# Optimization experiments

Hardware: AMD Instinct MI355X
Metric: run time of the kernel (lower is better)

Reference implementation:

```python
import jax, jax.numpy as jnp
import numpy as np
from jax import lax

B, C, H, W = 2, 3, 1024, 1024
SH, SW = 128, 128
FH, FW = H // SH, W // SW  # integer pooling factors (8, 8)
NPRE = 64
L = 0.24          # diffusion step size l
K = 0.03          # exp(log(0.03)), fixed logk for feature_extractor='none'
EPS = 1e-8
DEPS = 0.1


def _g(x):
    # g(x) = 1 / (1 + |x*x| / K^2)
    return 1.0 / (1.0 + (x * x) / (K * K))


def _conductance(feats):
    # cv: [B,1,H-1,W], ch: [B,1,H,W-1]; mean of |finite diff| over channels
    cv = _g(jnp.mean(jnp.abs(feats[:, :, 1:, :] - feats[:, :, :-1, :]), axis=1, keepdims=True))
    ch = _g(jnp.mean(jnp.abs(feats[:, :, :, 1:] - feats[:, :, :, :-1]), axis=1, keepdims=True))
    return cv, ch


def _downsample(x):
    # AdaptiveAvgPool2d((SH,SW)) with integer factor == exact mean pooling
    b = x.shape[0]
    return x.reshape(b, 1, SH, FH, SW, FW).mean(axis=(3, 5))


def _upsample(x):
    # F.interpolate(mode='nearest') with integer factor == pixel replication
    return jnp.repeat(jnp.repeat(x, FH, axis=2), FW, axis=3)


def setup_inputs() -> dict:
    key = jax.random.key(0)
    k1, k2, k3, k4 = jax.random.split(key, 4)
    guide = jax.random.normal(k1, (B, C, H, W), dtype=jnp.float32)
    y_bicubic = jax.random.uniform(k2, (B, 1, H, W), dtype=jnp.float32)
    source = jax.random.uniform(k3, (B, 1, SH, SW), dtype=jnp.float32)
    mask_lr = jax.random.uniform(k4, (B, 1, SH, SW), dtype=jnp.float32)
    return {"guide": guide, "y_bicubic": y_bicubic, "source": source, "mask_lr": mask_lr}


def _diffuse(img, guide, source, mask_inv):
    # feature_extractor == 'none': guide_feats = cat([guide, img], 1)
    feats = jnp.concatenate([guide, img], axis=1)
    cv, ch = _conductance(feats)

    def step(im, _):
        # diffuse_step: dv/dh computed from the SAME input image, then
        # vertical update applied first, horizontal second (matches torch in-place order)
        dv = im[:, :, 1:, :] - im[:, :, :-1, :]
        dh = im[:, :, :, 1:] - im[:, :, :, :-1]
        tv = L * cv * dv
        th = L * ch * dh
        im = im.at[:, :, 1:, :].add(-tv).at[:, :, :-1, :].add(tv)
        im = im.at[:, :, :, 1:].add(-th).at[:, :, :, :-1].add(th)
        # adjust_step: low-res ratio correction
        im_ss = _downsample(im)
        ratio_ss = jnp.where(mask_inv, 1.0, source / (im_ss + EPS))
        return im * _upsample(ratio_ss), None

    img, _ = lax.scan(step, img, None, length=NPRE)
    return img, cv, ch


def reference(guide, y_bicubic, source, mask_lr):
    # shift depths if min(source) <= deps (jit-safe scalar select)
    shift = jnp.where(jnp.min(source) <= DEPS, DEPS, 0.0).astype(source.dtype)
    source = source + shift
    img = y_bicubic + shift
    mask_inv = mask_lr < 0.5
    y_pred, cv, ch = _diffuse(img, guide, source, mask_inv)
    y_pred = y_pred - shift
    return y_pred, cv, ch
```

## Files before the change

### kernel.cpp

```cpp
#include <hip/hip_runtime.h>


#define BB 2
#define HH 1024
#define WW 1024
#define NPIX (HH * WW)
#define CVN (1023 * 1024)
#define SHW (128 * 128)
#define LL 0.24f
#define KK2 (0.03f * 0.03f)
#define EPSF 1e-8f
#define DEPSF 0.1f
#define NPRE 64
#define NB 512
#define TPB 256

typedef unsigned long long u64;
typedef unsigned int uint4v __attribute__((ext_vector_type(4)));
#define ROWPAR ((size_t)NB * 2 * 128)
#define COLPAR ((size_t)NB * 2 * 32)

__device__ inline void ust4(void* p, uint4v q) {
    asm volatile("global_store_dwordx4 %0, %1, off sc0 sc1" :: "v"(p), "v"(q) : "memory");
}
__device__ inline uint4v uld4(const void* p) {
    uint4v r;
    asm volatile("global_load_dwordx4 %0, %1, off sc0 sc1" : "=v"(r) : "v"(p) : "memory");
    return r;
}
__device__ inline void vwait() { asm volatile("s_waitcnt vmcnt(0)" ::: "memory"); }

__device__ inline void pub2(u64* p, float v0, float v1, unsigned s) {
    uint4v q;
    q.x = __float_as_uint(v0); q.y = s;
    q.z = __float_as_uint(v1); q.w = s;
    ust4(p, q);
}
__device__ inline bool tags_ok(uint4v a, uint4v b, unsigned s) {
    return a.y == s && a.w == s && b.y == s && b.w == s;
}
__device__ inline float4 vals_of(uint4v a, uint4v b) {
    return make_float4(__uint_as_float(a.x), __uint_as_float(a.z),
                       __uint_as_float(b.x), __uint_as_float(b.z));
}

__device__ inline float gfun(float d) { return 1.0f / (1.0f + (d * d) / KK2); }

#define BAR() do { asm volatile("s_waitcnt lgkmcnt(0)" ::: "memory"); \
                   __builtin_amdgcn_s_barrier();                      \
                   __builtin_amdgcn_sched_barrier(0); } while (0)

__launch_bounds__(TPB, 2)
__global__ void persist_kernel(const float* __restrict__ guide, const float* __restrict__ yb,
                               const float* __restrict__ src, const float* __restrict__ mask,
                               float* __restrict__ out, float* __restrict__ out_cv,
                               float* __restrict__ out_ch,
                               u64* __restrict__ bufRow, u64* __restrict__ bufCol) {
    __shared__ float tile[2][32 * 128];
    __shared__ float sm[4];
    int blk = blockIdx.x;
    int b = blk >> 8;
    int r = blk & 255;
    int tileY = r >> 3;
    int tileX = r & 7;
    int tid = threadIdx.x;
    int cyL = tid >> 5;
    int g = tid & 31;
    int wv = tid >> 6;
    int l0 = tid & 63;
    int lx0 = g * 4;
    int ly0 = cyL * 4;
    int gx = tileX * 128 + lx0;
    int gy = tileY * 32 + ly0;

    float mmin = 1e30f;
    const float4* s4 = (const float4*)src;
    for (int i = tid; i < (BB * SHW) / 4; i += TPB) {
        float4 v = s4[i];
        mmin = fminf(mmin, fminf(fminf(v.x, v.y), fminf(v.z, v.w)));
    }
    for (int off = 32; off > 0; off >>= 1) mmin = fminf(mmin, __shfl_down(mmin, off));
    if ((tid & 63) == 0) sm[tid >> 6] = mmin;
    __syncthreads();
    float mm = fminf(fminf(sm[0], sm[1]), fminf(sm[2], sm[3]));
    float shift = (mm <= DEPSF) ? DEPSF : 0.0f;

    int ry[6];
#pragma unroll
    for (int j = 0; j < 6; ++j) {
        int y = gy - 1 + j;
        ry[j] = y < 0 ? 0 : (y > 1023 ? 1023 : y);
    }
    int cxl = (gx > 0) ? gx - 1 : 0;
    int cxr = (gx + 4 < 1024) ? gx + 4 : 1023;
    float4 z4 = make_float4(0.f, 0.f, 0.f, 0.f);
    float4 vd[5] = {z4, z4, z4, z4, z4};
    float4 hd[4] = {z4, z4, z4, z4};
    float hmd[4] = {0.f, 0.f, 0.f, 0.f};
    float4 imv[4], r0v = z4, r5v = z4;
    float slv[4], srv[4];
#pragma unroll
    for (int c = 0; c < 4; ++c) {
        const float* F = (c < 3) ? guide + ((size_t)b * 3 + c) * NPIX
                                 : yb + (size_t)b * NPIX;
        float4 rr[6];
#pragma unroll
        for (int j = 0; j < 6; ++j)
            rr[j] = *(const float4*)(F + (size_t)ry[j] * WW + gx);
#pragma unroll
        for (int j = 0; j < 5; ++j) {
            vd[j].x += fabsf(rr[j + 1].x - rr[j].x);
            vd[j].y += fabsf(rr[j + 1].y - rr[j].y);
            vd[j].z += fabsf(rr[j + 1].z - rr[j].z);
            vd[j].w += fabsf(rr[j + 1].w - rr[j].w);
        }
#pragma unroll
        for (int k = 0; k < 4; ++k) {
            float4 R = rr[k + 1];
            float sr = F[(size_t)ry[k + 1] * WW + cxr];
            float sl = F[(size_t)ry[k + 1] * WW + cxl];
            hd[k].x += fabsf(R.y - R.x);
            hd[k].y += fabsf(R.z - R.y);
            hd[k].z += fabsf(R.w - R.z);
            hd[k].w += fabsf(sr - R.w);
            hmd[k] += fabsf(R.x - sl);
            if (c == 3) { imv[k] = R; slv[k] = sl; srv[k] = sr; }
        }
        if (c == 3) { r0v = rr[0]; r5v = rr[5]; }
    }
    float4 cvR[5], chR[4];
    float hmR[4];
#pragma unroll
    for (int j = 0; j < 5; ++j) {
        int y = gy - 1 + j;
        if (y < 0 || y > 1022) {
            cvR[j] = z4;
        } else {
            cvR[j] = make_float4(gfun(vd[j].x * 0.25f), gfun(vd[j].y * 0.25f),
                                 gfun(vd[j].z * 0.25f), gfun(vd[j].w * 0.25f));
        }
    }
#pragma unroll
    for (int k = 0; k < 4; ++k) {
        chR[k] = make_float4(gfun(hd[k].x * 0.25f), gfun(hd[k].y * 0.25f),
                             gfun(hd[k].z * 0.25f), gfun(hd[k].w * 0.25f));
        if (gx + 3 == 1023) chR[k].w = 0.f;
        hmR[k] = (gx > 0) ? gfun(hmd[k] * 0.25f) : 0.f;
    }
#pragma unroll
    for (int j = 1; j < 5; ++j) {
        int y = gy + j - 1;
        if (y <= 1022)
            *(float4*)(out_cv + (size_t)b * CVN + (size_t)y * WW + gx) = cvR[j];
    }
#pragma unroll
    for (int k = 0; k < 4; ++k) {
        float* base = out_ch + (size_t)b * CVN + (size_t)(gy + k) * 1023;
        base[gx + 0] = chR[k].x;
        base[gx + 1] = chR[k].y;
        base[gx + 2] = chR[k].z;
        if (gx + 3 < 1023) base[gx + 3] = chR[k].w;
    }

    int sidx = b * SHW + (tileY * 4 + (cyL >> 1)) * 128 + tileX * 16 + (g >> 1);
    float sval = src[sidx] + shift;
    bool masked = mask[sidx] < 0.5f;

    bool upAct = (cyL == 0 && tileY > 0);
    bool dnAct = (cyL == 7 && tileY < 31);
    bool lAct  = (g == 0  && tileX > 0);
    bool rAct  = (g == 31 && tileX < 7);
    bool pubTop = (wv == 0 && tileY > 0);
    bool pubBot = (wv == 3 && tileY < 31);

    float* cur = &tile[0][0];
    float* nxt = &tile[1][0];

#pragma unroll
    for (int k = 0; k < 4; ++k) {
        float4 v = imv[k];
        v.x += shift; v.y += shift; v.z += shift; v.w += shift;
        *(float4*)&cur[(ly0 + k) * 128 + lx0] = v;
    }
    float4 hUp = z4, hDn = z4;
    float xlR[4] = {0.f, 0.f, 0.f, 0.f}, xrR[4] = {0.f, 0.f, 0.f, 0.f};
    if (upAct) { hUp = r0v; hUp.x += shift; hUp.y += shift; hUp.z += shift; hUp.w += shift; }
    if (dnAct) { hDn = r5v; hDn.x += shift; hDn.y += shift; hDn.z += shift; hDn.w += shift; }
    if (lAct) {
#pragma unroll
        for (int k = 0; k < 4; ++k) xlR[k] = slv[k] + shift;
    }
    if (rAct) {
#pragma unroll
        for (int k = 0; k < 4; ++k) xrR[k] = srv[k] + shift;
    }
    __syncthreads();

    float4 nv[4];
    for (int t = 0; t < NPRE; ++t) {
        unsigned sP = (unsigned)t;
        size_t rOffP = (t & 1) ? ROWPAR : 0;
        size_t cOffP = (t & 1) ? COLPAR : 0;
        const u64* pUp = upAct ? &bufRow[rOffP + (((size_t)blk - 8) * 2 + 1) * 128 + lx0] : nullptr;
        const u64* pDn = dnAct ? &bufRow[rOffP + (((size_t)blk + 8) * 2 + 0) * 128 + lx0] : nullptr;
        const u64* pL  = lAct  ? &bufCol[cOffP + (((size_t)blk - 1) * 2 + 1) * 32 + ly0] : nullptr;
        const u64* pR  = rAct  ? &bufCol[cOffP + (((size_t)blk + 1) * 2 + 0) * 32 + ly0] : nullptr;
        uint4v uA, uB, dA, dB, lA, lB, rA, rB;
        bool pollRound = (t > 0);
        if (pollRound) {
            if (upAct) { uA = uld4(pUp); uB = uld4(pUp + 2); }
            if (dnAct) { dA = uld4(pDn); dB = uld4(pDn + 2); }
            if (lAct)  { lA = uld4(pL);  lB = uld4(pL + 2); }
            if (rAct)  { rA = uld4(pR);  rB = uld4(pR + 2); }
        }

        float4 rUp = (cyL == 0) ? z4 : *(float4*)&cur[(ly0 - 1) * 128 + lx0];
        float4 rC  = *(float4*)&cur[ly0 * 128 + lx0];
        float csum = 0.f;
#pragma unroll
        for (int k = 0; k < 4; ++k) {
            float4 rDn = (k == 3 && cyL == 7) ? z4
                       : *(float4*)&cur[(ly0 + 1 + k) * 128 + lx0];
            float4 cu = cvR[k], cd = cvR[k + 1], h4 = chR[k];
            float xs = __shfl_up(rC.w, 1);
            float xt = __shfl_down(rC.x, 1);
            float xl = (g == 0)  ? 0.f : xs;
            float xr = (g == 31) ? 0.f : xt;
            float hm = hmR[k];
            float4 a;
            a.x = rC.x + LL * (cd.x * (rDn.x - rC.x) - cu.x * (rC.x - rUp.x)
                             + h4.x * (rC.y - rC.x) - hm   * (rC.x - xl));
            a.y = rC.y + LL * (cd.y * (rDn.y - rC.y) - cu.y * (rC.y - rUp.y)
                             + h4.y * (rC.z - rC.y) - h4.x * (rC.y - rC.x));
            a.z = rC.z + LL * (cd.z * (rDn.z - rC.z) - cu.z * (rC.z - rUp.z)
                             + h4.z * (rC.w - rC.z) - h4.y * (rC.z - rC.y));
            a.w = rC.w + LL * (cd.w * (rDn.w - rC.w) - cu.w * (rC.w - rUp.w)
                             + h4.w * (xr   - rC.w) - h4.z * (rC.w - rC.z));
            nv[k] = a;
            csum += a.x + a.y + a.z + a.w;
            rUp = rC; rC = rDn;
        }

        if (pollRound) {
            vwait();
            bool needU = upAct, needD = dnAct, needL = lAct, needR = rAct;
            for (;;) {
                if (needU && tags_ok(uA, uB, sP)) { hUp = vals_of(uA, uB); needU = false; }
                if (needD && tags_ok(dA, dB, sP)) { hDn = vals_of(dA, dB); needD = false; }
                if (needL && tags_ok(lA, lB, sP)) {
                    float4 c = vals_of(lA, lB);
                    xlR[0] = c.x; xlR[1] = c.y; xlR[2] = c.z; xlR[3] = c.w;
                    needL = false;
                }
                if (needR && tags_ok(rA, rB, sP)) {
                    float4 c = vals_of(rA, rB);
                    xrR[0] = c.x; xrR[1] = c.y; xrR[2] = c.z; xrR[3] = c.w;
                    needR = false;
                }
                if (__all(!(needU || needD || needL || needR))) break;
                __builtin_amdgcn_s_sleep(1);
                if (needU) { uA = uld4(pUp); uB = uld4(pUp + 2); }
                if (needD) { dA = uld4(pDn); dB = uld4(pDn + 2); }
                if (needL) { lA = uld4(pL);  lB = uld4(pL + 2); }
                if (needR) { rA = uld4(pR);  rB = uld4(pR + 2); }
                vwait();
            }
        }

        float cadd = 0.f;
        if (cyL == 0) {
            float4 cu = cvR[0];
            float c0 = LL * cu.x * hUp.x, c1 = LL * cu.y * hUp.y;
            float c2 = LL * cu.z * hUp.z, c3 = LL * cu.w * hUp.w;
            nv[0].x += c0; nv[0].y += c1; nv[0].z += c2; nv[0].w += c3;
            cadd += c0 + c1 + c2 + c3;
        }
        if (cyL == 7) {
            float4 cd = cvR[4];
            float c0 = LL * cd.x * hDn.x, c1 = LL * cd.y * hDn.y;
            float c2 = LL * cd.z * hDn.z, c3 = LL * cd.w * hDn.w;
            nv[3].x += c0; nv[3].y += c1; nv[3].z += c2; nv[3].w += c3;
            cadd += c0 + c1 + c2 + c3;
        }
        if (g == 0) {
#pragma unroll
            for (int k = 0; k < 4; ++k) {
                float c = LL * hmR[k] * xlR[k];
                nv[k].x += c; cadd += c;
            }
        }
        if (g == 31) {
#pragma unroll
            for (int k = 0; k < 4; ++k) {
                float c = LL * chR[k].w * xrR[k];
                nv[k].w += c; cadd += c;
            }
        }
        csum += cadd;

        csum += __shfl_xor(csum, 1);
        csum += __shfl_xor(csum, 32);
        float ratio = masked ? 1.0f : sval / (csum * (1.0f / 64.0f) + EPSF);

        if (t == NPRE - 1) {
            float* ob = out + (size_t)b * NPIX;
#pragma unroll
            for (int k = 0; k < 4; ++k) {
                float4 v = nv[k];
                v.x = v.x * ratio - shift; v.y = v.y * ratio - shift;
                v.z = v.z * ratio - shift; v.w = v.w * ratio - shift;
                *(float4*)(ob + (size_t)(gy + k) * WW + gx) = v;
            }
            break;
        }
#pragma unroll
        for (int k = 0; k < 4; ++k) {
            nv[k].x *= ratio; nv[k].y *= ratio; nv[k].z *= ratio; nv[k].w *= ratio;
        }

        unsigned s2 = (unsigned)(t + 1);
        size_t rOff2 = (s2 & 1) ? ROWPAR : 0;
        size_t cOff2 = (s2 & 1) ? COLPAR : 0;
        if (pubTop) {
            float a = __shfl(nv[0].x, l0 >> 1), bq = __shfl(nv[0].y, l0 >> 1);
            float c = __shfl(nv[0].z, l0 >> 1), d = __shfl(nv[0].w, l0 >> 1);
            float v0 = (l0 & 1) ? c : a, v1 = (l0 & 1) ? d : bq;
            uint4v q; q.x = __float_as_uint(v0); q.y = s2;
            q.z = __float_as_uint(v1); q.w = s2;
            ust4(&bufRow[rOff2 + ((size_t)blk * 2 + 0) * 128 + 2 * l0], q);
        }
        if (pubBot) {
            int sl = 32 + (l0 >> 1);
            float a = __shfl(nv[3].x, sl), bq = __shfl(nv[3].y, sl);
            float c = __shfl(nv[3].z, sl), d = __shfl(nv[3].w, sl);
            float v0 = (l0 & 1) ? c : a, v1 = (l0 & 1) ? d : bq;
            uint4v q; q.x = __float_as_uint(v0); q.y = s2;
            q.z = __float_as_uint(v1); q.w = s2;
            ust4(&bufRow[rOff2 + ((size_t)blk * 2 + 1) * 128 + 2 * l0], q);
        }
        if (lAct) {
            u64* p = &bufCol[cOff2 + ((size_t)blk * 2 + 0) * 32 + ly0];
            pub2(p, nv[0].x, nv[1].x, s2);
            pub2(p + 2, nv[2].x, nv[3].x, s2);
        }
        if (rAct) {
            u64* p = &bufCol[cOff2 + ((size_t)blk * 2 + 1) * 32 + ly0];
            pub2(p, nv[0].w, nv[1].w, s2);
            pub2(p + 2, nv[2].w, nv[3].w, s2);
        }

#pragma unroll
        for (int k = 0; k < 4; ++k)
            *(float4*)&nxt[(ly0 + k) * 128 + lx0] = nv[k];
        BAR();
        float* tmp = cur; cur = nxt; nxt = tmp;
    }
}

extern "C" void kernel_launch(void* const* d_in, const int* in_sizes, int n_in,
                              void* d_out, int out_size, void* d_ws, size_t ws_size,
                              hipStream_t stream) {
    const float* guide = (const float*)d_in[0];
    const float* yb    = (const float*)d_in[1];
    const float* src   = (const float*)d_in[2];
    const float* mask  = (const float*)d_in[3];

    float* out    = (float*)d_out;
    float* out_cv = out + (size_t)BB * NPIX;
    float* out_ch = out_cv + (size_t)BB * CVN;

    u64* bufRow = (u64*)d_ws;
    u64* bufCol = bufRow + 2 * ROWPAR;

    persist_kernel<<<NB, TPB, 0, stream>>>(guide, yb, src, mask, out, out_cv,
                                           out_ch, bufRow, bufCol);
}
```

Baseline: 231.6 us.

## Use 64-row tiles with register-resident image and LDS boundary exchange

Halves the block count to 256 persistent blocks, each covering a 64x128 tile. Each thread now keeps 8 rows in registers, and only its first and last rows go through a small double-buffered LDS array instead of a full tile copy. This cuts per-step LDS traffic and the cross-block halo exchange per pixel, and each 8x8 pooling cell now sits within a thread pair, so one shuffle is dropped. The cost is higher register pressure, since launch bounds are relaxed to 1 block per SM, and less parallelism across CUs.

```diff
diff --git a/kernel.cpp b/kernel.cpp
--- a/kernel.cpp
+++ b/kernel.cpp
@@ -12,13 +12,13 @@
 #define EPSF 1e-8f
 #define DEPSF 0.1f
 #define NPRE 64
-#define NB 512
+#define NB 256
 #define TPB 256
 
 typedef unsigned long long u64;
 typedef unsigned int uint4v __attribute__((ext_vector_type(4)));
 #define ROWPAR ((size_t)NB * 2 * 128)
-#define COLPAR ((size_t)NB * 2 * 32)
+#define COLPAR ((size_t)NB * 2 * 64)
 
 __device__ inline void ust4(void* p, uint4v q) {
     asm volatile("global_store_dwordx4 %0, %1, off sc0 sc1" :: "v"(p), "v"(q) : "memory");
@@ -50,17 +50,17 @@
                    __builtin_amdgcn_s_barrier();                      \
                    __builtin_amdgcn_sched_barrier(0); } while (0)
 
-__launch_bounds__(TPB, 2)
+__launch_bounds__(TPB, 1)
 __global__ void persist_kernel(const float* __restrict__ guide, const float* __restrict__ yb,
                                const float* __restrict__ src, const float* __restrict__ mask,
                                float* __restrict__ out, float* __restrict__ out_cv,
                                float* __restrict__ out_ch,
                                u64* __restrict__ bufRow, u64* __restrict__ bufCol) {
-    __shared__ float tile[2][32 * 128];
+    __shared__ float bnd[2][8][2][128];
     __shared__ float sm[4];
     int blk = blockIdx.x;
-    int b = blk >> 8;
-    int r = blk & 255;
+    int b = blk >> 7;
+    int r = blk & 127;
     int tileY = r >> 3;
     int tileX = r & 7;
     int tid = threadIdx.x;
@@ -69,9 +69,9 @@
     int wv = tid >> 6;
     int l0 = tid & 63;
     int lx0 = g * 4;
-    int ly0 = cyL * 4;
+    int ly0 = cyL * 8;
     int gx = tileX * 128 + lx0;
-    int gy = tileY * 32 + ly0;
+    int gy = tileY * 64 + ly0;
 
     float mmin = 1e30f;
     const float4* s4 = (const float4*)src;
@@ -85,37 +85,37 @@
     float mm = fminf(fminf(sm[0], sm[1]), fminf(sm[2], sm[3]));
     float shift = (mm <= DEPSF) ? DEPSF : 0.0f;
 
-    int ry[6];
-#pragma unroll
-    for (int j = 0; j < 6; ++j) {
+    int ry[10];
+#pragma unroll
+    for (int j = 0; j < 10; ++j) {
         int y = gy - 1 + j;
         ry[j] = y < 0 ? 0 : (y > 1023 ? 1023 : y);
     }
     int cxl = (gx > 0) ? gx - 1 : 0;
     int cxr = (gx + 4 < 1024) ? gx + 4 : 1023;
     float4 z4 = make_float4(0.f, 0.f, 0.f, 0.f);
-    float4 vd[5] = {z4, z4, z4, z4, z4};
-    float4 hd[4] = {z4, z4, z4, z4};
-    float hmd[4] = {0.f, 0.f, 0.f, 0.f};
-    float4 imv[4], r0v = z4, r5v = z4;
-    float slv[4], srv[4];
+    float4 vd[9] = {z4, z4, z4, z4, z4, z4, z4, z4, z4};
+    float4 hd[8] = {z4, z4, z4, z4, z4, z4, z4, z4};
+    float hmd[8] = {0.f, 0.f, 0.f, 0.f, 0.f, 0.f, 0.f, 0.f};
+    float4 imv[8], r0v = z4, r9v = z4;
+    float slv[8], srv[8];
 #pragma unroll
     for (int c = 0; c < 4; ++c) {
         const float* F = (c < 3) ? guide + ((size_t)b * 3 + c) * NPIX
                                  : yb + (size_t)b * NPIX;
-        float4 rr[6];
-#pragma unroll
-        for (int j = 0; j < 6; ++j)
+        float4 rr[10];
+#pragma unroll
+        for (int j = 0; j < 10; ++j)
             rr[j] = *(const float4*)(F + (size_t)ry[j] * WW + gx);
 #pragma unroll
-        for (int j = 0; j < 5; ++j) {
+        for (int j = 0; j < 9; ++j) {
             vd[j].x += fabsf(rr[j + 1].x - rr[j].x);
             vd[j].y += fabsf(rr[j + 1].y - rr[j].y);
             vd[j].z += fabsf(rr[j + 1].z - rr[j].z);
             vd[j].w += fabsf(rr[j + 1].w - rr[j].w);
         }
 #pragma unroll
-        for (int k = 0; k < 4; ++k) {
+        for (int k = 0; k < 8; ++k) {
             float4 R = rr[k + 1];
             float sr = F[(size_t)ry[k + 1] * WW + cxr];
             float sl = F[(size_t)ry[k + 1] * WW + cxl];
@@ -126,12 +126,12 @@
             hmd[k] += fabsf(R.x - sl);
             if (c == 3) { imv[k] = R; slv[k] = sl; srv[k] = sr; }
         }
-        if (c == 3) { r0v = rr[0]; r5v = rr[5]; }
-    }
-    float4 cvR[5], chR[4];
-    float hmR[4];
-#pragma unroll
-    for (int j = 0; j < 5; ++j) {
+        if (c == 3) { r0v = rr[0]; r9v = rr[9]; }
+    }
+    float4 cvR[9], chR[8];
+    float hmR[8];
+#pragma unroll
+    for (int j = 0; j < 9; ++j) {
         int y = gy - 1 + j;
         if (y < 0 || y > 1022) {
             cvR[j] = z4;
@@ -141,20 +141,20 @@
         }
     }
 #pragma unroll
-    for (int k = 0; k < 4; ++k) {
+    for (int k = 0; k < 8; ++k) {
         chR[k] = make_float4(gfun(hd[k].x * 0.25f), gfun(hd[k].y * 0.25f),
                              gfun(hd[k].z * 0.25f), gfun(hd[k].w * 0.25f));
         if (gx + 3 == 1023) chR[k].w = 0.f;
         hmR[k] = (gx > 0) ? gfun(hmd[k] * 0.25f) : 0.f;
     }
 #pragma unroll
-    for (int j = 1; j < 5; ++j) {
+    for (int j = 1; j < 9; ++j) {
         int y = gy + j - 1;
         if (y <= 1022)
             *(float4*)(out_cv + (size_t)b * CVN + (size_t)y * WW + gx) = cvR[j];
     }
 #pragma unroll
-    for (int k = 0; k < 4; ++k) {
+    for (int k = 0; k < 8; ++k) {
         float* base = out_ch + (size_t)b * CVN + (size_t)(gy + k) * 1023;
         base[gx + 0] = chR[k].x;
         base[gx + 1] = chR[k].y;
@@ -162,83 +162,87 @@
         if (gx + 3 < 1023) base[gx + 3] = chR[k].w;
     }
 
-    int sidx = b * SHW + (tileY * 4 + (cyL >> 1)) * 128 + tileX * 16 + (g >> 1);
+    int sidx = b * SHW + (tileY * 8 + cyL) * 128 + tileX * 16 + (g >> 1);
     float sval = src[sidx] + shift;
     bool masked = mask[sidx] < 0.5f;
 
     bool upAct = (cyL == 0 && tileY > 0);
-    bool dnAct = (cyL == 7 && tileY < 31);
+    bool dnAct = (cyL == 7 && tileY < 15);
     bool lAct  = (g == 0  && tileX > 0);
     bool rAct  = (g == 31 && tileX < 7);
     bool pubTop = (wv == 0 && tileY > 0);
-    bool pubBot = (wv == 3 && tileY < 31);
-
-    float* cur = &tile[0][0];
-    float* nxt = &tile[1][0];
-
-#pragma unroll
-    for (int k = 0; k < 4; ++k) {
+    bool pubBot = (wv == 3 && tileY < 15);
+
+    float4 cur[8];
+#pragma unroll
+    for (int k = 0; k < 8; ++k) {
         float4 v = imv[k];
         v.x += shift; v.y += shift; v.z += shift; v.w += shift;
-        *(float4*)&cur[(ly0 + k) * 128 + lx0] = v;
+        cur[k] = v;
     }
     float4 hUp = z4, hDn = z4;
-    float xlR[4] = {0.f, 0.f, 0.f, 0.f}, xrR[4] = {0.f, 0.f, 0.f, 0.f};
+    float xlR[8] = {0.f, 0.f, 0.f, 0.f, 0.f, 0.f, 0.f, 0.f};
+    float xrR[8] = {0.f, 0.f, 0.f, 0.f, 0.f, 0.f, 0.f, 0.f};
     if (upAct) { hUp = r0v; hUp.x += shift; hUp.y += shift; hUp.z += shift; hUp.w += shift; }
-    if (dnAct) { hDn = r5v; hDn.x += shift; hDn.y += shift; hDn.z += shift; hDn.w += shift; }
+    if (dnAct) { hDn = r9v; hDn.x += shift; hDn.y += shift; hDn.z += shift; hDn.w += shift; }
     if (lAct) {
 #pragma unroll
-        for (int k = 0; k < 4; ++k) xlR[k] = slv[k] + shift;
+        for (int k = 0; k < 8; ++k) xlR[k] = slv[k] + shift;
     }
     if (rAct) {
 #pragma unroll
-        for (int k = 0; k < 4; ++k) xrR[k] = srv[k] + shift;
-    }
+        for (int k = 0; k < 8; ++k) xrR[k] = srv[k] + shift;
+    }
+    *(float4*)&bnd[0][cyL][0][lx0] = cur[0];
+    *(float4*)&bnd[0][cyL][1][lx0] = cur[7];
     __syncthreads();
 
-    float4 nv[4];
     for (int t = 0; t < NPRE; ++t) {
+        int par = t & 1;
         unsigned sP = (unsigned)t;
-        size_t rOffP = (t & 1) ? ROWPAR : 0;
-        size_t cOffP = (t & 1) ? COLPAR : 0;
+        size_t rOffP = par ? ROWPAR : 0;
+        size_t cOffP = par ? COLPAR : 0;
         const u64* pUp = upAct ? &bufRow[rOffP + (((size_t)blk - 8) * 2 + 1) * 128 + lx0] : nullptr;
         const u64* pDn = dnAct ? &bufRow[rOffP + (((size_t)blk + 8) * 2 + 0) * 128 + lx0] : nullptr;
-        const u64* pL  = lAct  ? &bufCol[cOffP + (((size_t)blk - 1) * 2 + 1) * 32 + ly0] : nullptr;
-        const u64* pR  = rAct  ? &bufCol[cOffP + (((size_t)blk + 1) * 2 + 0) * 32 + ly0] : nullptr;
-        uint4v uA, uB, dA, dB, lA, lB, rA, rB;
+        const u64* pL  = lAct  ? &bufCol[cOffP + (((size_t)blk - 1) * 2 + 1) * 64 + ly0] : nullptr;
+        const u64* pR  = rAct  ? &bufCol[cOffP + (((size_t)blk + 1) * 2 + 0) * 64 + ly0] : nullptr;
+        uint4v uA, uB, dA, dB, lA, lB, lC, lD, rA, rB, rC, rD;
         bool pollRound = (t > 0);
         if (pollRound) {
             if (upAct) { uA = uld4(pUp); uB = uld4(pUp + 2); }
             if (dnAct) { dA = uld4(pDn); dB = uld4(pDn + 2); }
-            if (lAct)  { lA = uld4(pL);  lB = uld4(pL + 2); }
-            if (rAct)  { rA = uld4(pR);  rB = uld4(pR + 2); }
-        }
-
-        float4 rUp = (cyL == 0) ? z4 : *(float4*)&cur[(ly0 - 1) * 128 + lx0];
-        float4 rC  = *(float4*)&cur[ly0 * 128 + lx0];
+            if (lAct)  { lA = uld4(pL);  lB = uld4(pL + 2); lC = uld4(pL + 4); lD = uld4(pL + 6); }
+            if (rAct)  { rA = uld4(pR);  rB = uld4(pR + 2); rC = uld4(pR + 4); rD = uld4(pR + 6); }
+        }
+
+        float4 ldsUp = z4, ldsDn = z4;
+        if (cyL > 0) ldsUp = *(float4*)&bnd[par][cyL - 1][1][lx0];
+        if (cyL < 7) ldsDn = *(float4*)&bnd[par][cyL + 1][0][lx0];
+
+        float4 pu = (cyL == 0) ? z4 : ldsUp;
+        float4 pc = cur[0];
         float csum = 0.f;
 #pragma unroll
-        for (int k = 0; k < 4; ++k) {
-            float4 rDn = (k == 3 && cyL == 7) ? z4
-                       : *(float4*)&cur[(ly0 + 1 + k) * 128 + lx0];
+        for (int k = 0; k < 8; ++k) {
+            float4 dn = (k == 7) ? ((cyL == 7) ? z4 : ldsDn) : cur[k + 1];
             float4 cu = cvR[k], cd = cvR[k + 1], h4 = chR[k];
-            float xs = __shfl_up(rC.w, 1);
-            float xt = __shfl_down(rC.x, 1);
+            float xs = __shfl_up(pc.w, 1);
+            float xt = __shfl_down(pc.x, 1);
             float xl = (g == 0)  ? 0.f : xs;
             float xr = (g == 31) ? 0.f : xt;
             float hm = hmR[k];
             float4 a;
-            a.x = rC.x + LL * (cd.x * (rDn.x - rC.x) - cu.x * (rC.x - rUp.x)
-                             + h4.x * (rC.y - rC.x) - hm   * (rC.x - xl));
-            a.y = rC.y + LL * (cd.y * (rDn.y - rC.y) - cu.y * (rC.y - rUp.y)
-                             + h4.y * (rC.z - rC.y) - h4.x * (rC.y - rC.x));
-            a.z = rC.z + LL * (cd.z * (rDn.z - rC.z) - cu.z * (rC.z - rUp.z)
-                             + h4.z * (rC.w - rC.z) - h4.y * (rC.z - rC.y));
-            a.w = rC.w + LL * (cd.w * (rDn.w - rC.w) - cu.w * (rC.w - rUp.w)
-                             + h4.w * (xr   - rC.w) - h4.z * (rC.w - rC.z));
-            nv[k] = a;
+            a.x = pc.x + LL * (cd.x * (dn.x - pc.x) - cu.x * (pc.x - pu.x)
+                             + h4.x * (pc.y - pc.x) - hm   * (pc.x - xl));
+            a.y = pc.y + LL * (cd.y * (dn.y - pc.y) - cu.y * (pc.y - pu.y)
+                             + h4.y * (pc.z - pc.y) - h4.x * (pc.y - pc.x));
+            a.z = pc.z + LL * (cd.z * (dn.z - pc.z) - cu.z * (pc.z - pu.z)
+                             + h4.z * (pc.w - pc.z) - h4.y * (pc.z - pc.y));
+            a.w = pc.w + LL * (cd.w * (dn.w - pc.w) - cu.w * (pc.w - pu.w)
+                             + h4.w * (xr   - pc.w) - h4.z * (pc.w - pc.z));
             csum += a.x + a.y + a.z + a.w;
-            rUp = rC; rC = rDn;
+            cur[k] = a;
+            pu = pc; pc = dn;
         }
 
         if (pollRound) {
@@ -247,22 +251,24 @@
             for (;;) {
                 if (needU && tags_ok(uA, uB, sP)) { hUp = vals_of(uA, uB); needU = false; }
                 if (needD && tags_ok(dA, dB, sP)) { hDn = vals_of(dA, dB); needD = false; }
-                if (needL && tags_ok(lA, lB, sP)) {
-                    float4 c = vals_of(lA, lB);
-                    xlR[0] = c.x; xlR[1] = c.y; xlR[2] = c.z; xlR[3] = c.w;
+                if (needL && tags_ok(lA, lB, sP) && tags_ok(lC, lD, sP)) {
+                    float4 c1 = vals_of(lA, lB), c2 = vals_of(lC, lD);
+                    xlR[0] = c1.x; xlR[1] = c1.y; xlR[2] = c1.z; xlR[3] = c1.w;
+                    xlR[4] = c2.x; xlR[5] = c2.y; xlR[6] = c2.z; xlR[7] = c2.w;
                     needL = false;
                 }
-                if (needR && tags_ok(rA, rB, sP)) {
-                    float4 c = vals_of(rA, rB);
-                    xrR[0] = c.x; xrR[1] = c.y; xrR[2] = c.z; xrR[3] = c.w;
+                if (needR && tags_ok(rA, rB, sP) && tags_ok(rC, rD, sP)) {
+                    float4 c1 = vals_of(rA, rB), c2 = vals_of(rC, rD);
+                    xrR[0] = c1.x; xrR[1] = c1.y; xrR[2] = c1.z; xrR[3] = c1.w;
+                    xrR[4] = c2.x; xrR[5] = c2.y; xrR[6] = c2.z; xrR[7] = c2.w;
                     needR = false;
                 }
                 if (__all(!(needU || needD || needL || needR))) break;
                 __builtin_amdgcn_s_sleep(1);
                 if (needU) { uA = uld4(pUp); uB = uld4(pUp + 2); }
                 if (needD) { dA = uld4(pDn); dB = uld4(pDn + 2); }
-                if (needL) { lA = uld4(pL);  lB = uld4(pL + 2); }
-                if (needR) { rA = uld4(pR);  rB = uld4(pR + 2); }
+                if (needL) { lA = uld4(pL);  lB = uld4(pL + 2); lC = uld4(pL + 4); lD = uld4(pL + 6); }
+                if (needR) { rA = uld4(pR);  rB = uld4(pR + 2); rC = uld4(pR + 4); rD = uld4(pR + 6); }
                 vwait();
             }
         }
@@ -272,41 +278,39 @@
             float4 cu = cvR[0];
             float c0 = LL * cu.x * hUp.x, c1 = LL * cu.y * hUp.y;
             float c2 = LL * cu.z * hUp.z, c3 = LL * cu.w * hUp.w;
-            nv[0].x += c0; nv[0].y += c1; nv[0].z += c2; nv[0].w += c3;
+            cur[0].x += c0; cur[0].y += c1; cur[0].z += c2; cur[0].w += c3;
             cadd += c0 + c1 + c2 + c3;
         }
         if (cyL == 7) {
-            float4 cd = cvR[4];
+            float4 cd = cvR[8];
             float c0 = LL * cd.x * hDn.x, c1 = LL * cd.y * hDn.y;
             float c2 = LL * cd.z * hDn.z, c3 = LL * cd.w * hDn.w;
-            nv[3].x += c0; nv[3].y += c1; nv[3].z += c2; nv[3].w += c3;
+            cur[7].x += c0; cur[7].y += c1; cur[7].z += c2; cur[7].w += c3;
             cadd += c0 + c1 + c2 + c3;
         }
         if (g == 0) {
 #pragma unroll
-            for (int k = 0; k < 4; ++k) {
+            for (int k = 0; k < 8; ++k) {
                 float c = LL * hmR[k] * xlR[k];
-                nv[k].x += c; cadd += c;
+                cur[k].x += c; cadd += c;
             }
         }
         if (g == 31) {
 #pragma unroll
-            for (int k = 0; k < 4; ++k) {
+            for (int k = 0; k < 8; ++k) {
                 float c = LL * chR[k].w * xrR[k];
-                nv[k].w += c; cadd += c;
+                cur[k].w += c; cadd += c;
             }
         }
         csum += cadd;
-
         csum += __shfl_xor(csum, 1);
-        csum += __shfl_xor(csum, 32);
         float ratio = masked ? 1.0f : sval / (csum * (1.0f / 64.0f) + EPSF);
 
         if (t == NPRE - 1) {
             float* ob = out + (size_t)b * NPIX;
 #pragma unroll
-            for (int k = 0; k < 4; ++k) {
-                float4 v = nv[k];
+            for (int k = 0; k < 8; ++k) {
+                float4 v = cur[k];
                 v.x = v.x * ratio - shift; v.y = v.y * ratio - shift;
                 v.z = v.z * ratio - shift; v.w = v.w * ratio - shift;
                 *(float4*)(ob + (size_t)(gy + k) * WW + gx) = v;
@@ -314,16 +318,16 @@
             break;
         }
 #pragma unroll
-        for (int k = 0; k < 4; ++k) {
-            nv[k].x *= ratio; nv[k].y *= ratio; nv[k].z *= ratio; nv[k].w *= ratio;
+        for (int k = 0; k < 8; ++k) {
+            cur[k].x *= ratio; cur[k].y *= ratio; cur[k].z *= ratio; cur[k].w *= ratio;
         }
 
         unsigned s2 = (unsigned)(t + 1);
         size_t rOff2 = (s2 & 1) ? ROWPAR : 0;
         size_t cOff2 = (s2 & 1) ? COLPAR : 0;
         if (pubTop) {
-            float a = __shfl(nv[0].x, l0 >> 1), bq = __shfl(nv[0].y, l0 >> 1);
-            float c = __shfl(nv[0].z, l0 >> 1), d = __shfl(nv[0].w, l0 >> 1);
+            float a = __shfl(cur[0].x, l0 >> 1), bq = __shfl(cur[0].y, l0 >> 1);
+            float c = __shfl(cur[0].z, l0 >> 1), d = __shfl(cur[0].w, l0 >> 1);
             float v0 = (l0 & 1) ? c : a, v1 = (l0 & 1) ? d : bq;
             uint4v q; q.x = __float_as_uint(v0); q.y = s2;
             q.z = __float_as_uint(v1); q.w = s2;
@@ -331,29 +335,31 @@
         }
         if (pubBot) {
             int sl = 32 + (l0 >> 1);
-            float a = __shfl(nv[3].x, sl), bq = __shfl(nv[3].y, sl);
-            float c = __shfl(nv[3].z, sl), d = __shfl(nv[3].w, sl);
+            float a = __shfl(cur[7].x, sl), bq = __shfl(cur[7].y, sl);
+            float c = __shfl(cur[7].z, sl), d = __shfl(cur[7].w, sl);
             float v0 = (l0 & 1) ? c : a, v1 = (l0 & 1) ? d : bq;
             uint4v q; q.x = __float_as_uint(v0); q.y = s2;
             q.z = __float_as_uint(v1); q.w = s2;
             ust4(&bufRow[rOff2 + ((size_t)blk * 2 + 1) * 128 + 2 * l0], q);
         }
         if (lAct) {
-            u64* p = &bufCol[cOff2 + ((size_t)blk * 2 + 0) * 32 + ly0];
-            pub2(p, nv[0].x, nv[1].x, s2);
-            pub2(p + 2, nv[2].x, nv[3].x, s2);
+            u64* p = &bufCol[cOff2 + ((size_t)blk * 2 + 0) * 64 + ly0];
+            pub2(p,     cur[0].x, cur[1].x, s2);
+            pub2(p + 2, cur[2].x, cur[3].x, s2);
+            pub2(p + 4, cur[4].x, cur[5].x, s2);
+            pub2(p + 6, cur[6].x, cur[7].x, s2);
         }
         if (rAct) {
-            u64* p = &bufCol[cOff2 + ((size_t)blk * 2 + 1) * 32 + ly0];
-            pub2(p, nv[0].w, nv[1].w, s2);
-            pub2(p + 2, nv[2].w, nv[3].w, s2);
-        }
-
-#pragma unroll
-        for (int k = 0; k < 4; ++k)
-            *(float4*)&nxt[(ly0 + k) * 128 + lx0] = nv[k];
+            u64* p = &bufCol[cOff2 + ((size_t)blk * 2 + 1) * 64 + ly0];
+            pub2(p,     cur[0].w, cur[1].w, s2);
+            pub2(p + 2, cur[2].w, cur[3].w, s2);
+            pub2(p + 4, cur[4].w, cur[5].w, s2);
+            pub2(p + 6, cur[6].w, cur[7].w, s2);
+        }
+
+        *(float4*)&bnd[par ^ 1][cyL][0][lx0] = cur[0];
+        *(float4*)&bnd[par ^ 1][cyL][1][lx0] = cur[7];
         BAR();
-        float* tmp = cur; cur = nxt; nxt = tmp;
     }
 }
 
```

Result: slower. 248.9 us (+7.5%).

## Use 64-row tiles with 512 threads and register-resident interior pixels

Applied to the files above, without the earlier changes.

Each block now covers a 64x128 tile with 512 threads, halving the number of blocks and the inter-block halo publish/poll traffic. The full LDS tile is replaced by register-resident 4x4 pixel patches, and only each thread's top and bottom rows go through a small double-buffered LDS boundary array. This cuts LDS traffic and halves the tile perimeter per pixel. The cost is a wider barrier across 8 waves and higher register pressure, and the persistent grid still depends on every block being co-resident.

```diff
diff --git a/kernel.cpp b/kernel.cpp
--- a/kernel.cpp
+++ b/kernel.cpp
@@ -12,13 +12,13 @@
 #define EPSF 1e-8f
 #define DEPSF 0.1f
 #define NPRE 64
-#define NB 512
-#define TPB 256
+#define NB 256
+#define TPB 512
 
 typedef unsigned long long u64;
 typedef unsigned int uint4v __attribute__((ext_vector_type(4)));
 #define ROWPAR ((size_t)NB * 2 * 128)
-#define COLPAR ((size_t)NB * 2 * 32)
+#define COLPAR ((size_t)NB * 2 * 64)
 
 __device__ inline void ust4(void* p, uint4v q) {
     asm volatile("global_store_dwordx4 %0, %1, off sc0 sc1" :: "v"(p), "v"(q) : "memory");
@@ -56,11 +56,11 @@
                                float* __restrict__ out, float* __restrict__ out_cv,
                                float* __restrict__ out_ch,
                                u64* __restrict__ bufRow, u64* __restrict__ bufCol) {
-    __shared__ float tile[2][32 * 128];
-    __shared__ float sm[4];
+    __shared__ float bnd[2][16][2][128];
+    __shared__ float sm[8];
     int blk = blockIdx.x;
-    int b = blk >> 8;
-    int r = blk & 255;
+    int b = blk >> 7;
+    int r = blk & 127;
     int tileY = r >> 3;
     int tileX = r & 7;
     int tid = threadIdx.x;
@@ -71,7 +71,7 @@
     int lx0 = g * 4;
     int ly0 = cyL * 4;
     int gx = tileX * 128 + lx0;
-    int gy = tileY * 32 + ly0;
+    int gy = tileY * 64 + ly0;
 
     float mmin = 1e30f;
     const float4* s4 = (const float4*)src;
@@ -82,7 +82,8 @@
     for (int off = 32; off > 0; off >>= 1) mmin = fminf(mmin, __shfl_down(mmin, off));
     if ((tid & 63) == 0) sm[tid >> 6] = mmin;
     __syncthreads();
-    float mm = fminf(fminf(sm[0], sm[1]), fminf(sm[2], sm[3]));
+    float mm = fminf(fminf(fminf(sm[0], sm[1]), fminf(sm[2], sm[3])),
+                     fminf(fminf(sm[4], sm[5]), fminf(sm[6], sm[7])));
     float shift = (mm <= DEPSF) ? DEPSF : 0.0f;
 
     int ry[6];
@@ -162,25 +163,23 @@
         if (gx + 3 < 1023) base[gx + 3] = chR[k].w;
     }
 
-    int sidx = b * SHW + (tileY * 4 + (cyL >> 1)) * 128 + tileX * 16 + (g >> 1);
+    int sidx = b * SHW + (tileY * 8 + (cyL >> 1)) * 128 + tileX * 16 + (g >> 1);
     float sval = src[sidx] + shift;
     bool masked = mask[sidx] < 0.5f;
 
-    bool upAct = (cyL == 0 && tileY > 0);
-    bool dnAct = (cyL == 7 && tileY < 31);
+    bool upAct = (cyL == 0  && tileY > 0);
+    bool dnAct = (cyL == 15 && tileY < 15);
     bool lAct  = (g == 0  && tileX > 0);
     bool rAct  = (g == 31 && tileX < 7);
     bool pubTop = (wv == 0 && tileY > 0);
-    bool pubBot = (wv == 3 && tileY < 31);
-
-    float* cur = &tile[0][0];
-    float* nxt = &tile[1][0];
-
+    bool pubBot = (wv == 7 && tileY < 15);
+
+    float4 cur[4];
 #pragma unroll
     for (int k = 0; k < 4; ++k) {
         float4 v = imv[k];
         v.x += shift; v.y += shift; v.z += shift; v.w += shift;
-        *(float4*)&cur[(ly0 + k) * 128 + lx0] = v;
+        cur[k] = v;
     }
     float4 hUp = z4, hDn = z4;
     float xlR[4] = {0.f, 0.f, 0.f, 0.f}, xrR[4] = {0.f, 0.f, 0.f, 0.f};
@@ -194,17 +193,19 @@
 #pragma unroll
         for (int k = 0; k < 4; ++k) xrR[k] = srv[k] + shift;
     }
+    *(float4*)&bnd[0][cyL][0][lx0] = cur[0];
+    *(float4*)&bnd[0][cyL][1][lx0] = cur[3];
     __syncthreads();
 
-    float4 nv[4];
     for (int t = 0; t < NPRE; ++t) {
+        int par = t & 1;
         unsigned sP = (unsigned)t;
-        size_t rOffP = (t & 1) ? ROWPAR : 0;
-        size_t cOffP = (t & 1) ? COLPAR : 0;
+        size_t rOffP = par ? ROWPAR : 0;
+        size_t cOffP = par ? COLPAR : 0;
         const u64* pUp = upAct ? &bufRow[rOffP + (((size_t)blk - 8) * 2 + 1) * 128 + lx0] : nullptr;
         const u64* pDn = dnAct ? &bufRow[rOffP + (((size_t)blk + 8) * 2 + 0) * 128 + lx0] : nullptr;
-        const u64* pL  = lAct  ? &bufCol[cOffP + (((size_t)blk - 1) * 2 + 1) * 32 + ly0] : nullptr;
-        const u64* pR  = rAct  ? &bufCol[cOffP + (((size_t)blk + 1) * 2 + 0) * 32 + ly0] : nullptr;
+        const u64* pL  = lAct  ? &bufCol[cOffP + (((size_t)blk - 1) * 2 + 1) * 64 + ly0] : nullptr;
+        const u64* pR  = rAct  ? &bufCol[cOffP + (((size_t)blk + 1) * 2 + 0) * 64 + ly0] : nullptr;
         uint4v uA, uB, dA, dB, lA, lB, rA, rB;
         bool pollRound = (t > 0);
         if (pollRound) {
@@ -214,31 +215,34 @@
             if (rAct)  { rA = uld4(pR);  rB = uld4(pR + 2); }
         }
 
-        float4 rUp = (cyL == 0) ? z4 : *(float4*)&cur[(ly0 - 1) * 128 + lx0];
-        float4 rC  = *(float4*)&cur[ly0 * 128 + lx0];
+        float4 ldsUp = z4, ldsDn = z4;
+        if (cyL > 0)  ldsUp = *(float4*)&bnd[par][cyL - 1][1][lx0];
+        if (cyL < 15) ldsDn = *(float4*)&bnd[par][cyL + 1][0][lx0];
+
+        float4 pu = (cyL == 0) ? z4 : ldsUp;
+        float4 pc = cur[0];
         float csum = 0.f;
 #pragma unroll
         for (int k = 0; k < 4; ++k) {
-            float4 rDn = (k == 3 && cyL == 7) ? z4
-                       : *(float4*)&cur[(ly0 + 1 + k) * 128 + lx0];
+            float4 dn = (k == 3) ? ((cyL == 15) ? z4 : ldsDn) : cur[k + 1];
             float4 cu = cvR[k], cd = cvR[k + 1], h4 = chR[k];
-            float xs = __shfl_up(rC.w, 1);
-            float xt = __shfl_down(rC.x, 1);
+            float xs = __shfl_up(pc.w, 1);
+            float xt = __shfl_down(pc.x, 1);
             float xl = (g == 0)  ? 0.f : xs;
             float xr = (g == 31) ? 0.f : xt;
             float hm = hmR[k];
             float4 a;
-            a.x = rC.x + LL * (cd.x * (rDn.x - rC.x) - cu.x * (rC.x - rUp.x)
-                             + h4.x * (rC.y - rC.x) - hm   * (rC.x - xl));
-            a.y = rC.y + LL * (cd.y * (rDn.y - rC.y) - cu.y * (rC.y - rUp.y)
-                             + h4.y * (rC.z - rC.y) - h4.x * (rC.y - rC.x));
-            a.z = rC.z + LL * (cd.z * (rDn.z - rC.z) - cu.z * (rC.z - rUp.z)
-                             + h4.z * (rC.w - rC.z) - h4.y * (rC.z - rC.y));
-            a.w = rC.w + LL * (cd.w * (rDn.w - rC.w) - cu.w * (rC.w - rUp.w)
-                             + h4.w * (xr   - rC.w) - h4.z * (rC.w - rC.z));
-            nv[k] = a;
+            a.x = pc.x + LL * (cd.x * (dn.x - pc.x) - cu.x * (pc.x - pu.x)
+                             + h4.x * (pc.y - pc.x) - hm   * (pc.x - xl));
+            a.y = pc.y + LL * (cd.y * (dn.y - pc.y) - cu.y * (pc.y - pu.y)
+                             + h4.y * (pc.z - pc.y) - h4.x * (pc.y - pc.x));
+            a.z = pc.z + LL * (cd.z * (dn.z - pc.z) - cu.z * (pc.z - pu.z)
+                             + h4.z * (pc.w - pc.z) - h4.y * (pc.z - pc.y));
+            a.w = pc.w + LL * (cd.w * (dn.w - pc.w) - cu.w * (pc.w - pu.w)
+                             + h4.w * (xr   - pc.w) - h4.z * (pc.w - pc.z));
             csum += a.x + a.y + a.z + a.w;
-            rUp = rC; rC = rDn;
+            cur[k] = a;
+            pu = pc; pc = dn;
         }
 
         if (pollRound) {
@@ -272,32 +276,31 @@
             float4 cu = cvR[0];
             float c0 = LL * cu.x * hUp.x, c1 = LL * cu.y * hUp.y;
             float c2 = LL * cu.z * hUp.z, c3 = LL * cu.w * hUp.w;
-            nv[0].x += c0; nv[0].y += c1; nv[0].z += c2; nv[0].w += c3;
+            cur[0].x += c0; cur[0].y += c1; cur[0].z += c2; cur[0].w += c3;
             cadd += c0 + c1 + c2 + c3;
         }
-        if (cyL == 7) {
+        if (cyL == 15) {
             float4 cd = cvR[4];
             float c0 = LL * cd.x * hDn.x, c1 = LL * cd.y * hDn.y;
             float c2 = LL * cd.z * hDn.z, c3 = LL * cd.w * hDn.w;
-            nv[3].x += c0; nv[3].y += c1; nv[3].z += c2; nv[3].w += c3;
+            cur[3].x += c0; cur[3].y += c1; cur[3].z += c2; cur[3].w += c3;
             cadd += c0 + c1 + c2 + c3;
         }
         if (g == 0) {
 #pragma unroll
             for (int k = 0; k < 4; ++k) {
                 float c = LL * hmR[k] * xlR[k];
-                nv[k].x += c; cadd += c;
+                cur[k].x += c; cadd += c;
             }
         }
         if (g == 31) {
 #pragma unroll
             for (int k = 0; k < 4; ++k) {
                 float c = LL * chR[k].w * xrR[k];
-                nv[k].w += c; cadd += c;
+                cur[k].w += c; cadd += c;
             }
         }
         csum += cadd;
-
         csum += __shfl_xor(csum, 1);
         csum += __shfl_xor(csum, 32);
         float ratio = masked ? 1.0f : sval / (csum * (1.0f / 64.0f) + EPSF);
@@ -306,7 +309,7 @@
             float* ob = out + (size_t)b * NPIX;
 #pragma unroll
             for (int k = 0; k < 4; ++k) {
-                float4 v = nv[k];
+                float4 v = cur[k];
                 v.x = v.x * ratio - shift; v.y = v.y * ratio - shift;
                 v.z = v.z * ratio - shift; v.w = v.w * ratio - shift;
                 *(float4*)(ob + (size_t)(gy + k) * WW + gx) = v;
@@ -315,15 +318,15 @@
         }
 #pragma unroll
         for (int k = 0; k < 4; ++k) {
-            nv[k].x *= ratio; nv[k].y *= ratio; nv[k].z *= ratio; nv[k].w *= ratio;
+            cur[k].x *= ratio; cur[k].y *= ratio; cur[k].z *= ratio; cur[k].w *= ratio;
         }
 
         unsigned s2 = (unsigned)(t + 1);
         size_t rOff2 = (s2 & 1) ? ROWPAR : 0;
         size_t cOff2 = (s2 & 1) ? COLPAR : 0;
         if (pubTop) {
-            float a = __shfl(nv[0].x, l0 >> 1), bq = __shfl(nv[0].y, l0 >> 1);
-            float c = __shfl(nv[0].z, l0 >> 1), d = __shfl(nv[0].w, l0 >> 1);
+            float a = __shfl(cur[0].x, l0 >> 1), bq = __shfl(cur[0].y, l0 >> 1);
+            float c = __shfl(cur[0].z, l0 >> 1), d = __shfl(cur[0].w, l0 >> 1);
             float v0 = (l0 & 1) ? c : a, v1 = (l0 & 1) ? d : bq;
             uint4v q; q.x = __float_as_uint(v0); q.y = s2;
             q.z = __float_as_uint(v1); q.w = s2;
@@ -331,29 +334,27 @@
         }
         if (pubBot) {
             int sl = 32 + (l0 >> 1);
-            float a = __shfl(nv[3].x, sl), bq = __shfl(nv[3].y, sl);
-            float c = __shfl(nv[3].z, sl), d = __shfl(nv[3].w, sl);
+            float a = __shfl(cur[3].x, sl), bq = __shfl(cur[3].y, sl);
+            float c = __shfl(cur[3].z, sl), d = __shfl(cur[3].w, sl);
             float v0 = (l0 & 1) ? c : a, v1 = (l0 & 1) ? d : bq;
             uint4v q; q.x = __float_as_uint(v0); q.y = s2;
             q.z = __float_as_uint(v1); q.w = s2;
             ust4(&bufRow[rOff2 + ((size_t)blk * 2 + 1) * 128 + 2 * l0], q);
         }
         if (lAct) {
-            u64* p = &bufCol[cOff2 + ((size_t)blk * 2 + 0) * 32 + ly0];
-            pub2(p, nv[0].x, nv[1].x, s2);
-            pub2(p + 2, nv[2].x, nv[3].x, s2);
+            u64* p = &bufCol[cOff2 + ((size_t)blk * 2 + 0) * 64 + ly0];
+            pub2(p,     cur[0].x, cur[1].x, s2);
+            pub2(p + 2, cur[2].x, cur[3].x, s2);
         }
         if (rAct) {
-            u64* p = &bufCol[cOff2 + ((size_t)blk * 2 + 1) * 32 + ly0];
-            pub2(p, nv[0].w, nv[1].w, s2);
-            pub2(p + 2, nv[2].w, nv[3].w, s2);
-        }
-
-#pragma unroll
-        for (int k = 0; k < 4; ++k)
-            *(float4*)&nxt[(ly0 + k) * 128 + lx0] = nv[k];
+            u64* p = &bufCol[cOff2 + ((size_t)blk * 2 + 1) * 64 + ly0];
+            pub2(p,     cur[0].w, cur[1].w, s2);
+            pub2(p + 2, cur[2].w, cur[3].w, s2);
+        }
+
+        *(float4*)&bnd[par ^ 1][cyL][0][lx0] = cur[0];
+        *(float4*)&bnd[par ^ 1][cyL][1][lx0] = cur[3];
         BAR();
-        float* tmp = cur; cur = nxt; nxt = tmp;
     }
 }
 
```

After: 219.6 us. 5.2% less time.
